# Optimization experiments

Measured on AMD Instinct MI355X. Metric: run time of the kernel, lower is better.

## Reference

```python
import jax, jax.numpy as jnp
import numpy as np
import math

B, LQ, LK = 2, 2048, 2048
DIM = 1024
H = 16
DH = DIM // H


def setup_inputs() -> dict:
    key = jax.random.key(0)
    ks = jax.random.split(key, 12)
    s = 1.0 / math.sqrt(DIM)
    return {
        "query": jax.random.normal(ks[0], (B, LQ, DIM), jnp.float32),
        "key": jax.random.normal(ks[1], (B, LK, DIM), jnp.float32),
        "value": jax.random.normal(ks[2], (B, LK, DIM), jnp.float32),
        "mask": jnp.zeros((B, LQ, LK), dtype=bool),
        "Wq": jax.random.normal(ks[3], (DIM, DIM), jnp.float32) * s,
        "bq": jax.random.normal(ks[4], (DIM,), jnp.float32) * s,
        "Wk": jax.random.normal(ks[5], (DIM, DIM), jnp.float32) * s,
        "bk": jax.random.normal(ks[6], (DIM,), jnp.float32) * s,
        "Wv": jax.random.normal(ks[7], (DIM, DIM), jnp.float32) * s,
        "bv": jax.random.normal(ks[8], (DIM,), jnp.float32) * s,
        "Wo": jax.random.normal(ks[9], (DIM, DIM), jnp.float32) * s,
        "bo": jax.random.normal(ks[10], (DIM,), jnp.float32) * s,
    }


def reference(query, key, value, mask, Wq, bq, Wk, bk, Wv, bv, Wo, bo):
    b = query.shape[0]

    def shape(x):  # (b, l, dim) -> (b, h, l, dh)
        return x.reshape(b, -1, H, DH).transpose(0, 2, 1, 3)

    q = shape(query @ Wq.T + bq)
    k = shape(key @ Wk.T + bk)
    v = shape(value @ Wv.T + bv)

    q = q / math.sqrt(DH)
    # (b, h, lq, lk) score matrix, computed in float32 as the original does
    scores = jnp.einsum("bhqd,bhkd->bhqk", q, k).astype(jnp.float32)
    scores = jnp.where(mask[:, None, :, :], jnp.float32(-1e18), scores)
    attn = jax.nn.softmax(scores, axis=-1).astype(q.dtype)
    context = jnp.einsum("bhqk,bhkd->bhqd", attn, v)
    context = context.transpose(0, 2, 1, 3).reshape(b, -1, H * DH)
    return context @ Wo.T + bo
```

## Files before the change

### kernel.cpp

```cpp
#include <hip/hip_runtime.h>
#include <hip/hip_bf16.h>

typedef __attribute__((ext_vector_type(4))) float float4v;
typedef __attribute__((ext_vector_type(8))) __bf16 bf16x8;
typedef __attribute__((ext_vector_type(4))) unsigned short ushort4v;
typedef __attribute__((ext_vector_type(8))) unsigned short ushort8v;

#define MFMA16(a, b, c) __builtin_amdgcn_mfma_f32_16x16x32_bf16(a, b, c, 0, 0, 0)

__device__ __forceinline__ unsigned short f2bf(float f) {
    return __builtin_bit_cast(unsigned short, (__bf16)f);
}

__device__ __forceinline__ float fast_exp2(float x) {
#if __has_builtin(__builtin_amdgcn_exp2f)
    return __builtin_amdgcn_exp2f(x);
#else
    return exp2f(x);
#endif
}

__device__ __forceinline__ void gl_lds16(const unsigned short* g, unsigned short* l) {
    __builtin_amdgcn_global_load_lds(
        (const __attribute__((address_space(1))) void*)g,
        (__attribute__((address_space(3))) void*)l, 16, 0, 0);
}

__device__ __forceinline__ void bar_raw() {
    __builtin_amdgcn_sched_barrier(0);
    __builtin_amdgcn_s_barrier();
    __builtin_amdgcn_sched_barrier(0);
}

__device__ __forceinline__ void sbar() { __builtin_amdgcn_sched_barrier(0); }

struct CvtSeg { const float* s; unsigned short* d; int n; };
struct Cvt4 { CvtSeg seg[4]; };

__global__ __launch_bounds__(256) void cvt_kernel(Cvt4 a) {
    const CvtSeg c = a.seg[blockIdx.y];
    const int stride = gridDim.x * 256 * 8;
    for (int i = (blockIdx.x * 256 + threadIdx.x) * 8; i < c.n; i += stride) {
        float4v v0 = *(const float4v*)(c.s + i);
        float4v v1 = *(const float4v*)(c.s + i + 4);
        ushort8v u;
        u[0] = f2bf(v0.x); u[1] = f2bf(v0.y); u[2] = f2bf(v0.z); u[3] = f2bf(v0.w);
        u[4] = f2bf(v1.x); u[5] = f2bf(v1.y); u[6] = f2bf(v1.z); u[7] = f2bf(v1.w);
        *(ushort8v*)(c.d + i) = u;
    }
}

__global__ __launch_bounds__(256) void gemm_qkv_kernel(
    const float* qa, const float* ka, const float* va,
    const unsigned short* Wqb, const unsigned short* Wkb, const unsigned short* Wvb,
    const float* bq, const float* bk, const float* bv,
    unsigned short* Qb, unsigned short* Kb, unsigned short* Vb, float qscale) {
    __shared__ unsigned short As[2][128 * 64];
    __shared__ unsigned short Ws[2][128 * 64];
    const int id = blockIdx.x;
    const int work = (id & 7) * 96 + (id >> 3);
    const int x = work & 31;
    const int combo = work >> 5;
    const int y = combo & 7;
    const int z = combo >> 3;
    const float* A = z == 0 ? qa : (z == 1 ? ka : va);
    const unsigned short* W = z == 0 ? Wqb : (z == 1 ? Wkb : Wvb);
    const float* bias = z == 0 ? bq : (z == 1 ? bk : bv);
    unsigned short* Cout = z == 0 ? Qb : (z == 1 ? Kb : Vb);
    const float scale = z == 0 ? qscale : 1.0f;
    const int m0 = x * 128, n0 = y * 128;
    const int N = 1024, K = 1024;

    const int t = threadIdx.x;
    const int w = t >> 6, lane = t & 63;
    const int quad = lane >> 4, l16 = lane & 15;
    const int wm = (w >> 1) * 64, wn = (w & 1) * 64;

    float4v acc[4][4];
    for (int i = 0; i < 4; ++i)
        for (int j = 0; j < 4; ++j) acc[i][j] = float4v{0.f, 0.f, 0.f, 0.f};

    const int srow = lane >> 3;
    const int scol = (lane & 7) * 8;

    float4v faA[4][2], faB[4][2];

#define LOAD_A(dst, tile)                                                     \
    _Pragma("unroll") for (int i = 0; i < 4; ++i) {                           \
        const int c = w * 4 + i;                                              \
        const float* s_ = A + (size_t)(m0 + c * 8 + srow) * K + (tile) * 64 + scol; \
        dst[i][0] = *(const float4v*)s_;                                      \
        dst[i][1] = *(const float4v*)(s_ + 4);                                \
    }
#define STAGE_W(buf, tile)                                                    \
    _Pragma("unroll") for (int i = 0; i < 4; ++i) {                           \
        const int c = w * 4 + i;                                              \
        gl_lds16(W + (size_t)(n0 + c * 8 + srow) * K + (tile) * 64 + scol,    \
                 &Ws[buf][c * 512 + lane * 8]);                               \
    }
#define WRITE_A(buf, src)                                                     \
    _Pragma("unroll") for (int i = 0; i < 4; ++i) {                           \
        const int c = w * 4 + i;                                              \
        ushort8v u;                                                           \
        u[0] = f2bf(src[i][0].x); u[1] = f2bf(src[i][0].y);                   \
        u[2] = f2bf(src[i][0].z); u[3] = f2bf(src[i][0].w);                   \
        u[4] = f2bf(src[i][1].x); u[5] = f2bf(src[i][1].y);                   \
        u[6] = f2bf(src[i][1].z); u[7] = f2bf(src[i][1].w);                   \
        *(ushort8v*)&As[buf][c * 512 + lane * 8] = u;                         \
    }
#define MFMA_PHASE(buf)                                                       \
    for (int ks = 0; ks < 2; ++ks) {                                          \
        bf16x8 af[4], wf[4];                                                  \
        for (int i = 0; i < 4; ++i)                                           \
            af[i] = *(const bf16x8*)&As[buf][(wm + i * 16 + l16) * 64 + ks * 32 + quad * 8]; \
        for (int i = 0; i < 4; ++i)                                           \
            wf[i] = *(const bf16x8*)&Ws[buf][(wn + i * 16 + l16) * 64 + ks * 32 + quad * 8]; \
        for (int mi = 0; mi < 4; ++mi)                                        \
            for (int ni = 0; ni < 4; ++ni)                                    \
                acc[mi][ni] = MFMA16(af[mi], wf[ni], acc[mi][ni]);            \
    }

    STAGE_W(0, 0);
    sbar();
    LOAD_A(faA, 0);
    LOAD_A(faB, 1);
    WRITE_A(0, faA);
    sbar();
    asm volatile("s_waitcnt vmcnt(8) lgkmcnt(0)" ::: "memory");
    bar_raw();

    for (int kk = 0; kk < 8; ++kk) {
        const int te = kk * 2;
        {
            const int ta = (te + 2 < 16) ? te + 2 : 15;
            STAGE_W(1, te + 1);
            sbar();
            LOAD_A(faA, ta);
            WRITE_A(1, faB);
            MFMA_PHASE(0);
            sbar();
            asm volatile("s_waitcnt vmcnt(8) lgkmcnt(0)" ::: "memory");
            bar_raw();
        }
        {
            const int to = te + 1;
            const int tw = (to + 1 < 16) ? to + 1 : 15;
            const int ta = (to + 2 < 16) ? to + 2 : 15;
            STAGE_W(0, tw);
            sbar();
            LOAD_A(faB, ta);
            WRITE_A(0, faA);
            MFMA_PHASE(1);
            sbar();
            asm volatile("s_waitcnt vmcnt(8) lgkmcnt(0)" ::: "memory");
            bar_raw();
        }
    }
#undef LOAD_A
#undef STAGE_W
#undef WRITE_A
#undef MFMA_PHASE

    for (int mi = 0; mi < 4; ++mi)
        for (int ni = 0; ni < 4; ++ni) {
            const int col = n0 + wn + ni * 16 + l16;
            const float bv = bias[col];
            for (int reg = 0; reg < 4; ++reg) {
                const int row = m0 + wm + mi * 16 + quad * 4 + reg;
                Cout[(size_t)row * N + col] = f2bf((acc[mi][ni][reg] + bv) * scale);
            }
        }
}

__global__ __launch_bounds__(256) void gemm_out_kernel(const unsigned short* __restrict__ A,
                                                       const unsigned short* __restrict__ W,
                                                       const float* __restrict__ bias,
                                                       float* __restrict__ Cout) {
    __shared__ unsigned short As[2][64 * 64];
    __shared__ unsigned short Ws[2][128 * 64];
    const int N = 1024, K = 1024;
    const int t = threadIdx.x;
    const int w = t >> 6, lane = t & 63;
    const int quad = lane >> 4, l16 = lane & 15;
    const int m0 = blockIdx.x * 64, n0 = blockIdx.y * 128;
    const int wm = (w & 1) * 32, wn = (w >> 1) * 64;

    float4v acc[2][4];
    for (int i = 0; i < 2; ++i)
        for (int j = 0; j < 4; ++j) acc[i][j] = float4v{0.f, 0.f, 0.f, 0.f};

    const int srow = lane >> 3;
    const int scol = (lane & 7) * 8;

#define STAGE(buf, tile)                                                      \
    _Pragma("unroll") for (int i = 0; i < 2; ++i) {                           \
        const int c = w * 2 + i;                                              \
        gl_lds16(A + (size_t)(m0 + c * 8 + srow) * K + (tile) * 64 + scol,    \
                 &As[buf][c * 512 + lane * 8]);                               \
    }                                                                         \
    _Pragma("unroll") for (int i = 0; i < 4; ++i) {                           \
        const int c = w * 4 + i;                                              \
        gl_lds16(W + (size_t)(n0 + c * 8 + srow) * K + (tile) * 64 + scol,    \
                 &Ws[buf][c * 512 + lane * 8]);                               \
    }
#define MFMA_PHASE(buf)                                                       \
    for (int ks = 0; ks < 2; ++ks) {                                          \
        bf16x8 af[2], wf[4];                                                  \
        for (int i = 0; i < 2; ++i)                                           \
            af[i] = *(const bf16x8*)&As[buf][(wm + i * 16 + l16) * 64 + ks * 32 + quad * 8]; \
        for (int i = 0; i < 4; ++i)                                           \
            wf[i] = *(const bf16x8*)&Ws[buf][(wn + i * 16 + l16) * 64 + ks * 32 + quad * 8]; \
        for (int mi = 0; mi < 2; ++mi)                                        \
            for (int ni = 0; ni < 4; ++ni)                                    \
                acc[mi][ni] = MFMA16(af[mi], wf[ni], acc[mi][ni]);            \
    }

    STAGE(0, 0);
    sbar();
    asm volatile("s_waitcnt vmcnt(0)" ::: "memory");
    bar_raw();

    for (int kk = 0; kk < 8; ++kk) {
        const int te = kk * 2;
        {
            STAGE(1, te + 1);
            MFMA_PHASE(0);
            sbar();
            asm volatile("s_waitcnt vmcnt(0) lgkmcnt(0)" ::: "memory");
            bar_raw();
        }
        {
            const int tw = (te + 2 < 16) ? te + 2 : 15;
            STAGE(0, tw);
            MFMA_PHASE(1);
            sbar();
            asm volatile("s_waitcnt vmcnt(0) lgkmcnt(0)" ::: "memory");
            bar_raw();
        }
    }
#undef STAGE
#undef MFMA_PHASE

    for (int mi = 0; mi < 2; ++mi)
        for (int ni = 0; ni < 4; ++ni) {
            const int col = n0 + wn + ni * 16 + l16;
            const float bv = bias[col];
            for (int reg = 0; reg < 4; ++reg) {
                const int row = m0 + wm + mi * 16 + quad * 4 + reg;
                Cout[(size_t)row * N + col] = acc[mi][ni][reg] + bv;
            }
        }
}

__global__ __launch_bounds__(256) void attn_kernel(const unsigned short* __restrict__ Q,
                                                   const unsigned short* __restrict__ Kg,
                                                   const unsigned short* __restrict__ Vg,
                                                   const unsigned char* __restrict__ mask,
                                                   unsigned short* __restrict__ Ctx) {
    const int bid = blockIdx.x;
    const int bh = bid & 31;
    const int qt = bid >> 5;
    const int b = bh >> 4, h = bh & 15;
    const int t = threadIdx.x, w = t >> 6, lane = t & 63;
    const int quad = lane >> 4, l16 = lane & 15;

    __shared__ unsigned short Pt[128][72];
    __shared__ unsigned short Ks[64][72];
    __shared__ unsigned short Vt[64][72];

    const unsigned short* Qp = Q + ((size_t)(b * 2048 + qt * 128)) * 1024 + h * 64;
    const unsigned short* Kp = Kg + ((size_t)b * 2048) * 1024 + h * 64;
    const unsigned short* Vp = Vg + ((size_t)b * 2048) * 1024 + h * 64;
    const unsigned char* Mp = mask + (size_t)(b * 2048 + qt * 128) * 2048;

    for (int p = 0; p < 4; ++p) {
        const int idx = t + p * 256;
        const int r = idx >> 3, c8 = (idx & 7) * 8;
        *(uint4*)&Pt[r][c8] = *(const uint4*)(Qp + (size_t)r * 1024 + c8);
    }
    __syncthreads();
    bf16x8 qf[2][2];
    for (int c = 0; c < 2; ++c)
        for (int ks = 0; ks < 2; ++ks)
            qf[c][ks] = *(const bf16x8*)&Pt[w * 32 + c * 16 + l16][ks * 32 + quad * 8];

    float4v o[2][4];
    for (int c = 0; c < 2; ++c)
        for (int i = 0; i < 4; ++i) o[c][i] = float4v{0.f, 0.f, 0.f, 0.f};
    float l_acc[2] = {0.f, 0.f};

    const int sr = t >> 3, sc8 = (t & 7) * 8;
    const int vkk = (t & 31) * 2, vd0 = (t >> 5) * 8;
    const int mrow = w * 32 + (lane >> 1);
    const int mc0 = (lane & 1) * 32;

    uint4 kreg0, kreg1, vreg0, vreg1, mreg0, mreg1;
    {
        kreg0 = *(const uint4*)(Kp + (size_t)sr * 1024 + sc8);
        kreg1 = *(const uint4*)(Kp + (size_t)(sr + 32) * 1024 + sc8);
        vreg0 = *(const uint4*)(Vp + (size_t)vkk * 1024 + vd0);
        vreg1 = *(const uint4*)(Vp + (size_t)(vkk + 1) * 1024 + vd0);
        mreg0 = *(const uint4*)(Mp + (size_t)mrow * 2048 + mc0);
        mreg1 = *(const uint4*)(Mp + (size_t)mrow * 2048 + mc0 + 16);
    }

    for (int kc = 0; kc < 2048; kc += 64) {
        __syncthreads();
        *(uint4*)&Ks[sr][sc8] = kreg0;
        *(uint4*)&Ks[sr + 32][sc8] = kreg1;
        {
            const unsigned short* pa = (const unsigned short*)&vreg0;
            const unsigned short* pb = (const unsigned short*)&vreg1;
            for (int j = 0; j < 8; ++j)
                *(unsigned int*)&Vt[vd0 + j][vkk] =
                    (unsigned int)pa[j] | ((unsigned int)pb[j] << 16);
        }
        const unsigned int mor = mreg0.x | mreg0.y | mreg0.z | mreg0.w |
                                 mreg1.x | mreg1.y | mreg1.z | mreg1.w;
        const bool anymask = __any(mor != 0);
        __syncthreads();

        const int kn = kc + 64;
        if (kn < 2048) {
            kreg0 = *(const uint4*)(Kp + (size_t)(kn + sr) * 1024 + sc8);
            kreg1 = *(const uint4*)(Kp + (size_t)(kn + sr + 32) * 1024 + sc8);
            vreg0 = *(const uint4*)(Vp + (size_t)(kn + vkk) * 1024 + vd0);
            vreg1 = *(const uint4*)(Vp + (size_t)(kn + vkk + 1) * 1024 + vd0);
            mreg0 = *(const uint4*)(Mp + (size_t)mrow * 2048 + kn + mc0);
            mreg1 = *(const uint4*)(Mp + (size_t)mrow * 2048 + kn + mc0 + 16);
        }

        float4v s0[4], s1[4];
        for (int nt = 0; nt < 4; ++nt) {
            const float4v z4 = float4v{0.f, 0.f, 0.f, 0.f};
            bf16x8 kf = *(const bf16x8*)&Ks[nt * 16 + l16][quad * 8];
            s0[nt] = MFMA16(kf, qf[0][0], z4);
            s1[nt] = MFMA16(kf, qf[1][0], z4);
            kf = *(const bf16x8*)&Ks[nt * 16 + l16][32 + quad * 8];
            s0[nt] = MFMA16(kf, qf[0][1], s0[nt]);
            s1[nt] = MFMA16(kf, qf[1][1], s1[nt]);
        }

        for (int ks = 0; ks < 2; ++ks) {
            for (int c = 0; c < 2; ++c) {
                float4v* s = c ? s1 : s0;
                const int qrow = w * 32 + c * 16 + l16;
                float lc = l_acc[c];
                for (int nt = ks * 2; nt < ks * 2 + 2; ++nt) {
                    float p0 = s[nt][0], p1 = s[nt][1], p2 = s[nt][2], p3 = s[nt][3];
                    if (anymask) {
                        const unsigned char* mr =
                            Mp + (size_t)qrow * 2048 + kc + nt * 16 + quad * 4;
                        if (mr[0]) p0 = -1e18f;
                        if (mr[1]) p1 = -1e18f;
                        if (mr[2]) p2 = -1e18f;
                        if (mr[3]) p3 = -1e18f;
                    }
                    const float e0 = fast_exp2(p0), e1 = fast_exp2(p1);
                    const float e2 = fast_exp2(p2), e3 = fast_exp2(p3);
                    lc += (e0 + e1) + (e2 + e3);
                    uint2 u;
                    u.x = (unsigned int)f2bf(e0) | ((unsigned int)f2bf(e1) << 16);
                    u.y = (unsigned int)f2bf(e2) | ((unsigned int)f2bf(e3) << 16);
                    *(uint2*)&Pt[qrow][nt * 16 + quad * 4] = u;
                }
                l_acc[c] = lc;
            }
            bf16x8 pf0 = *(const bf16x8*)&Pt[w * 32 + l16][ks * 32 + quad * 8];
            bf16x8 pf1 = *(const bf16x8*)&Pt[w * 32 + 16 + l16][ks * 32 + quad * 8];
            for (int dt = 0; dt < 4; ++dt) {
                bf16x8 vf = *(const bf16x8*)&Vt[dt * 16 + l16][ks * 32 + quad * 8];
                o[0][dt] = MFMA16(pf0, vf, o[0][dt]);
                o[1][dt] = MFMA16(pf1, vf, o[1][dt]);
            }
        }
    }

    float lfull[2];
    for (int c = 0; c < 2; ++c) {
        float l = l_acc[c];
        l += __shfl_xor(l, 16);
        l += __shfl_xor(l, 32);
        lfull[c] = l;
    }

    for (int c = 0; c < 2; ++c) {
        float inv[4];
        for (int reg = 0; reg < 4; ++reg)
            inv[reg] = 1.0f / __shfl(lfull[c], (lane & 48) | (quad * 4 + reg));
        for (int dt = 0; dt < 4; ++dt) {
            const int dcol = dt * 16 + l16;
            for (int reg = 0; reg < 4; ++reg) {
                const int ql = w * 32 + c * 16 + quad * 4 + reg;
                Ctx[((size_t)(b * 2048 + qt * 128 + ql)) * 1024 + h * 64 + dcol] =
                    f2bf(o[c][dt][reg] * inv[reg]);
            }
        }
    }
}

extern "C" void kernel_launch(void* const* d_in, const int* in_sizes, int n_in,
                              void* d_out, int out_size, void* d_ws, size_t ws_size,
                              hipStream_t stream) {
    (void)in_sizes; (void)n_in; (void)out_size; (void)ws_size;
    const float* query = (const float*)d_in[0];
    const float* key   = (const float*)d_in[1];
    const float* value = (const float*)d_in[2];
    const unsigned char* mask = (const unsigned char*)d_in[3];
    const float* Wq = (const float*)d_in[4];
    const float* bq = (const float*)d_in[5];
    const float* Wk = (const float*)d_in[6];
    const float* bk = (const float*)d_in[7];
    const float* Wv = (const float*)d_in[8];
    const float* bv = (const float*)d_in[9];
    const float* Wo = (const float*)d_in[10];
    const float* bo = (const float*)d_in[11];

    const size_t MD = (size_t)4096 * 1024;
    const size_t WD = (size_t)1024 * 1024;

    unsigned short* Qb  = (unsigned short*)d_ws;
    unsigned short* Kb  = Qb + MD;
    unsigned short* Vb  = Kb + MD;
    unsigned short* Wqb = Vb + MD;
    unsigned short* Wkb = Wqb + WD;
    unsigned short* Wvb = Wkb + WD;
    unsigned short* Wob = Wvb + WD;
    unsigned short* Cb  = Wob + WD;

    Cvt4 cv;
    cv.seg[0] = {Wq, Wqb, (int)WD};
    cv.seg[1] = {Wk, Wkb, (int)WD};
    cv.seg[2] = {Wv, Wvb, (int)WD};
    cv.seg[3] = {Wo, Wob, (int)WD};
    cvt_kernel<<<dim3(512, 4), 256, 0, stream>>>(cv);

    const float qscale = 0.125f * 1.44269504088896f;
    gemm_qkv_kernel<<<dim3(768), 256, 0, stream>>>(
        query, key, value, Wqb, Wkb, Wvb, bq, bk, bv, Qb, Kb, Vb, qscale);

    attn_kernel<<<dim3(512), 256, 0, stream>>>(Qb, Kb, Vb, mask, Cb);

    gemm_out_kernel<<<dim3(64, 8), 256, 0, stream>>>(Cb, Wob, bo, (float*)d_out);
}
```

Baseline: 275.8 us.

## Fuse weight fp32-to-bf16 conversion into GEMM loads and drop convert kernel

```diff
diff --git a/kernel.cpp b/kernel.cpp
--- a/kernel.cpp
+++ b/kernel.cpp
@@ -34,25 +34,9 @@
 
 __device__ __forceinline__ void sbar() { __builtin_amdgcn_sched_barrier(0); }
 
-struct CvtSeg { const float* s; unsigned short* d; int n; };
-struct Cvt4 { CvtSeg seg[4]; };
-
-__global__ __launch_bounds__(256) void cvt_kernel(Cvt4 a) {
-    const CvtSeg c = a.seg[blockIdx.y];
-    const int stride = gridDim.x * 256 * 8;
-    for (int i = (blockIdx.x * 256 + threadIdx.x) * 8; i < c.n; i += stride) {
-        float4v v0 = *(const float4v*)(c.s + i);
-        float4v v1 = *(const float4v*)(c.s + i + 4);
-        ushort8v u;
-        u[0] = f2bf(v0.x); u[1] = f2bf(v0.y); u[2] = f2bf(v0.z); u[3] = f2bf(v0.w);
-        u[4] = f2bf(v1.x); u[5] = f2bf(v1.y); u[6] = f2bf(v1.z); u[7] = f2bf(v1.w);
-        *(ushort8v*)(c.d + i) = u;
-    }
-}
-
 __global__ __launch_bounds__(256) void gemm_qkv_kernel(
     const float* qa, const float* ka, const float* va,
-    const unsigned short* Wqb, const unsigned short* Wkb, const unsigned short* Wvb,
+    const float* Wqf, const float* Wkf, const float* Wvf,
     const float* bq, const float* bk, const float* bv,
     unsigned short* Qb, unsigned short* Kb, unsigned short* Vb, float qscale) {
     __shared__ unsigned short As[2][128 * 64];
@@ -64,7 +48,7 @@
     const int y = combo & 7;
     const int z = combo >> 3;
     const float* A = z == 0 ? qa : (z == 1 ? ka : va);
-    const unsigned short* W = z == 0 ? Wqb : (z == 1 ? Wkb : Wvb);
+    const float* W = z == 0 ? Wqf : (z == 1 ? Wkf : Wvf);
     const float* bias = z == 0 ? bq : (z == 1 ? bk : bv);
     unsigned short* Cout = z == 0 ? Qb : (z == 1 ? Kb : Vb);
     const float scale = z == 0 ? qscale : 1.0f;
@@ -83,22 +67,16 @@
     const int srow = lane >> 3;
     const int scol = (lane & 7) * 8;
 
-    float4v faA[4][2], faB[4][2];
-
-#define LOAD_A(dst, tile)                                                     \
+    float4v faA[4][2], faB[4][2], fwA[4][2], fwB[4][2];
+
+#define LOADP(dst, P, base, tile)                                             \
     _Pragma("unroll") for (int i = 0; i < 4; ++i) {                           \
         const int c = w * 4 + i;                                              \
-        const float* s_ = A + (size_t)(m0 + c * 8 + srow) * K + (tile) * 64 + scol; \
+        const float* s_ = (P) + (size_t)((base) + c * 8 + srow) * K + (tile) * 64 + scol; \
         dst[i][0] = *(const float4v*)s_;                                      \
         dst[i][1] = *(const float4v*)(s_ + 4);                                \
     }
-#define STAGE_W(buf, tile)                                                    \
-    _Pragma("unroll") for (int i = 0; i < 4; ++i) {                           \
-        const int c = w * 4 + i;                                              \
-        gl_lds16(W + (size_t)(n0 + c * 8 + srow) * K + (tile) * 64 + scol,    \
-                 &Ws[buf][c * 512 + lane * 8]);                               \
-    }
-#define WRITE_A(buf, src)                                                     \
+#define WRITEP(arr, buf, src)                                                 \
     _Pragma("unroll") for (int i = 0; i < 4; ++i) {                           \
         const int c = w * 4 + i;                                              \
         ushort8v u;                                                           \
@@ -106,7 +84,7 @@
         u[2] = f2bf(src[i][0].z); u[3] = f2bf(src[i][0].w);                   \
         u[4] = f2bf(src[i][1].x); u[5] = f2bf(src[i][1].y);                   \
         u[6] = f2bf(src[i][1].z); u[7] = f2bf(src[i][1].w);                   \
-        *(ushort8v*)&As[buf][c * 512 + lane * 8] = u;                         \
+        *(ushort8v*)&arr[buf][c * 512 + lane * 8] = u;                        \
     }
 #define MFMA_PHASE(buf)                                                       \
     for (int ks = 0; ks < 2; ++ks) {                                          \
@@ -120,45 +98,36 @@
                 acc[mi][ni] = MFMA16(af[mi], wf[ni], acc[mi][ni]);            \
     }
 
-    STAGE_W(0, 0);
+    LOADP(faA, A, m0, 0); LOADP(fwA, W, n0, 0);
+    LOADP(faB, A, m0, 1); LOADP(fwB, W, n0, 1);
+    WRITEP(As, 0, faA); WRITEP(Ws, 0, fwA);
     sbar();
-    LOAD_A(faA, 0);
-    LOAD_A(faB, 1);
-    WRITE_A(0, faA);
-    sbar();
-    asm volatile("s_waitcnt vmcnt(8) lgkmcnt(0)" ::: "memory");
+    asm volatile("s_waitcnt lgkmcnt(0)" ::: "memory");
     bar_raw();
 
     for (int kk = 0; kk < 8; ++kk) {
         const int te = kk * 2;
         {
             const int ta = (te + 2 < 16) ? te + 2 : 15;
-            STAGE_W(1, te + 1);
-            sbar();
-            LOAD_A(faA, ta);
-            WRITE_A(1, faB);
+            LOADP(faA, A, m0, ta); LOADP(fwA, W, n0, ta);
+            WRITEP(As, 1, faB); WRITEP(Ws, 1, fwB);
             MFMA_PHASE(0);
             sbar();
-            asm volatile("s_waitcnt vmcnt(8) lgkmcnt(0)" ::: "memory");
+            asm volatile("s_waitcnt lgkmcnt(0)" ::: "memory");
             bar_raw();
         }
         {
-            const int to = te + 1;
-            const int tw = (to + 1 < 16) ? to + 1 : 15;
-            const int ta = (to + 2 < 16) ? to + 2 : 15;
-            STAGE_W(0, tw);
-            sbar();
-            LOAD_A(faB, ta);
-            WRITE_A(0, faA);
+            const int ta = (te + 3 < 16) ? te + 3 : 15;
+            LOADP(faB, A, m0, ta); LOADP(fwB, W, n0, ta);
+            WRITEP(As, 0, faA); WRITEP(Ws, 0, fwA);
             MFMA_PHASE(1);
             sbar();
-            asm volatile("s_waitcnt vmcnt(8) lgkmcnt(0)" ::: "memory");
+            asm volatile("s_waitcnt lgkmcnt(0)" ::: "memory");
             bar_raw();
         }
     }
-#undef LOAD_A
-#undef STAGE_W
-#undef WRITE_A
+#undef LOADP
+#undef WRITEP
 #undef MFMA_PHASE
 
     for (int mi = 0; mi < 4; ++mi)
@@ -173,7 +142,7 @@
 }
 
 __global__ __launch_bounds__(256) void gemm_out_kernel(const unsigned short* __restrict__ A,
-                                                       const unsigned short* __restrict__ W,
+                                                       const float* __restrict__ W,
                                                        const float* __restrict__ bias,
                                                        float* __restrict__ Cout) {
     __shared__ unsigned short As[2][64 * 64];
@@ -192,16 +161,30 @@
     const int srow = lane >> 3;
     const int scol = (lane & 7) * 8;
 
-#define STAGE(buf, tile)                                                      \
+    float4v fwA[4][2], fwB[4][2];
+
+#define STAGE_A(buf, tile)                                                    \
     _Pragma("unroll") for (int i = 0; i < 2; ++i) {                           \
         const int c = w * 2 + i;                                              \
         gl_lds16(A + (size_t)(m0 + c * 8 + srow) * K + (tile) * 64 + scol,    \
                  &As[buf][c * 512 + lane * 8]);                               \
-    }                                                                         \
+    }
+#define LOAD_W(dst, tile)                                                     \
     _Pragma("unroll") for (int i = 0; i < 4; ++i) {                           \
         const int c = w * 4 + i;                                              \
-        gl_lds16(W + (size_t)(n0 + c * 8 + srow) * K + (tile) * 64 + scol,    \
-                 &Ws[buf][c * 512 + lane * 8]);                               \
+        const float* s_ = W + (size_t)(n0 + c * 8 + srow) * K + (tile) * 64 + scol; \
+        dst[i][0] = *(const float4v*)s_;                                      \
+        dst[i][1] = *(const float4v*)(s_ + 4);                                \
+    }
+#define WRITE_W(buf, src)                                                     \
+    _Pragma("unroll") for (int i = 0; i < 4; ++i) {                           \
+        const int c = w * 4 + i;                                              \
+        ushort8v u;                                                           \
+        u[0] = f2bf(src[i][0].x); u[1] = f2bf(src[i][0].y);                   \
+        u[2] = f2bf(src[i][0].z); u[3] = f2bf(src[i][0].w);                   \
+        u[4] = f2bf(src[i][1].x); u[5] = f2bf(src[i][1].y);                   \
+        u[6] = f2bf(src[i][1].z); u[7] = f2bf(src[i][1].w);                   \
+        *(ushort8v*)&Ws[buf][c * 512 + lane * 8] = u;                         \
     }
 #define MFMA_PHASE(buf)                                                       \
     for (int ks = 0; ks < 2; ++ks) {                                          \
@@ -215,30 +198,44 @@
                 acc[mi][ni] = MFMA16(af[mi], wf[ni], acc[mi][ni]);            \
     }
 
-    STAGE(0, 0);
+    STAGE_A(0, 0);
     sbar();
-    asm volatile("s_waitcnt vmcnt(0)" ::: "memory");
+    LOAD_W(fwA, 0);
+    LOAD_W(fwB, 1);
+    WRITE_W(0, fwA);
+    sbar();
+    asm volatile("s_waitcnt lgkmcnt(0)" ::: "memory");
     bar_raw();
 
     for (int kk = 0; kk < 8; ++kk) {
         const int te = kk * 2;
         {
-            STAGE(1, te + 1);
+            const int ta = (te + 2 < 16) ? te + 2 : 15;
+            STAGE_A(1, te + 1);
+            sbar();
+            LOAD_W(fwA, ta);
+            WRITE_W(1, fwB);
             MFMA_PHASE(0);
             sbar();
-            asm volatile("s_waitcnt vmcnt(0) lgkmcnt(0)" ::: "memory");
+            asm volatile("s_waitcnt vmcnt(8) lgkmcnt(0)" ::: "memory");
             bar_raw();
         }
         {
-            const int tw = (te + 2 < 16) ? te + 2 : 15;
-            STAGE(0, tw);
+            const int tsA = (te + 2 < 16) ? te + 2 : 15;
+            const int ta = (te + 3 < 16) ? te + 3 : 15;
+            STAGE_A(0, tsA);
+            sbar();
+            LOAD_W(fwB, ta);
+            WRITE_W(0, fwA);
             MFMA_PHASE(1);
             sbar();
-            asm volatile("s_waitcnt vmcnt(0) lgkmcnt(0)" ::: "memory");
+            asm volatile("s_waitcnt vmcnt(8) lgkmcnt(0)" ::: "memory");
             bar_raw();
         }
     }
-#undef STAGE
+#undef STAGE_A
+#undef LOAD_W
+#undef WRITE_W
 #undef MFMA_PHASE
 
     for (int mi = 0; mi < 2; ++mi)
@@ -341,31 +338,32 @@
             s1[nt] = MFMA16(kf, qf[1][1], s1[nt]);
         }
 
+        for (int c = 0; c < 2; ++c) {
+            float4v* s = c ? s1 : s0;
+            const int qrow = w * 32 + c * 16 + l16;
+            float lc = l_acc[c];
+            for (int nt = 0; nt < 4; ++nt) {
+                float p0 = s[nt][0], p1 = s[nt][1], p2 = s[nt][2], p3 = s[nt][3];
+                if (anymask) {
+                    const unsigned char* mr =
+                        Mp + (size_t)qrow * 2048 + kc + nt * 16 + quad * 4;
+                    if (mr[0]) p0 = -1e18f;
+                    if (mr[1]) p1 = -1e18f;
+                    if (mr[2]) p2 = -1e18f;
+                    if (mr[3]) p3 = -1e18f;
+                }
+                const float e0 = fast_exp2(p0), e1 = fast_exp2(p1);
+                const float e2 = fast_exp2(p2), e3 = fast_exp2(p3);
+                lc += (e0 + e1) + (e2 + e3);
+                uint2 u;
+                u.x = (unsigned int)f2bf(e0) | ((unsigned int)f2bf(e1) << 16);
+                u.y = (unsigned int)f2bf(e2) | ((unsigned int)f2bf(e3) << 16);
+                *(uint2*)&Pt[qrow][nt * 16 + quad * 4] = u;
+            }
+            l_acc[c] = lc;
+        }
+
         for (int ks = 0; ks < 2; ++ks) {
-            for (int c = 0; c < 2; ++c) {
-                float4v* s = c ? s1 : s0;
-                const int qrow = w * 32 + c * 16 + l16;
-                float lc = l_acc[c];
-                for (int nt = ks * 2; nt < ks * 2 + 2; ++nt) {
-                    float p0 = s[nt][0], p1 = s[nt][1], p2 = s[nt][2], p3 = s[nt][3];
-                    if (anymask) {
-                        const unsigned char* mr =
-                            Mp + (size_t)qrow * 2048 + kc + nt * 16 + quad * 4;
-                        if (mr[0]) p0 = -1e18f;
-                        if (mr[1]) p1 = -1e18f;
-                        if (mr[2]) p2 = -1e18f;
-                        if (mr[3]) p3 = -1e18f;
-                    }
-                    const float e0 = fast_exp2(p0), e1 = fast_exp2(p1);
-                    const float e2 = fast_exp2(p2), e3 = fast_exp2(p3);
-                    lc += (e0 + e1) + (e2 + e3);
-                    uint2 u;
-                    u.x = (unsigned int)f2bf(e0) | ((unsigned int)f2bf(e1) << 16);
-                    u.y = (unsigned int)f2bf(e2) | ((unsigned int)f2bf(e3) << 16);
-                    *(uint2*)&Pt[qrow][nt * 16 + quad * 4] = u;
-                }
-                l_acc[c] = lc;
-            }
             bf16x8 pf0 = *(const bf16x8*)&Pt[w * 32 + l16][ks * 32 + quad * 8];
             bf16x8 pf1 = *(const bf16x8*)&Pt[w * 32 + 16 + l16][ks * 32 + quad * 8];
             for (int dt = 0; dt < 4; ++dt) {
@@ -417,29 +415,17 @@
     const float* bo = (const float*)d_in[11];
 
     const size_t MD = (size_t)4096 * 1024;
-    const size_t WD = (size_t)1024 * 1024;
-
-    unsigned short* Qb  = (unsigned short*)d_ws;
-    unsigned short* Kb  = Qb + MD;
-    unsigned short* Vb  = Kb + MD;
-    unsigned short* Wqb = Vb + MD;
-    unsigned short* Wkb = Wqb + WD;
-    unsigned short* Wvb = Wkb + WD;
-    unsigned short* Wob = Wvb + WD;
-    unsigned short* Cb  = Wob + WD;
-
-    Cvt4 cv;
-    cv.seg[0] = {Wq, Wqb, (int)WD};
-    cv.seg[1] = {Wk, Wkb, (int)WD};
-    cv.seg[2] = {Wv, Wvb, (int)WD};
-    cv.seg[3] = {Wo, Wob, (int)WD};
-    cvt_kernel<<<dim3(512, 4), 256, 0, stream>>>(cv);
+
+    unsigned short* Qb = (unsigned short*)d_ws;
+    unsigned short* Kb = Qb + MD;
+    unsigned short* Vb = Kb + MD;
+    unsigned short* Cb = Vb + MD;
 
     const float qscale = 0.125f * 1.44269504088896f;
     gemm_qkv_kernel<<<dim3(768), 256, 0, stream>>>(
-        query, key, value, Wqb, Wkb, Wvb, bq, bk, bv, Qb, Kb, Vb, qscale);
+        query, key, value, Wq, Wk, Wv, bq, bk, bv, Qb, Kb, Vb, qscale);
 
     attn_kernel<<<dim3(512), 256, 0, stream>>>(Qb, Kb, Vb, mask, Cb);
 
-    gemm_out_kernel<<<dim3(64, 8), 256, 0, stream>>>(Cb, Wob, bo, (float*)d_out);
-}
+    gemm_out_kernel<<<dim3(64, 8), 256, 0, stream>>>(Cb, Wo, bo, (float*)d_out);
+}
```

Result: slower. 282.5 us (+2.4%).
